# Kernel optimization log

Measured on AMD Instinct MI355X. Metric: run time of the kernel, lower is better.

## Reference

```python
import jax, jax.numpy as jnp
import numpy as np

B, LQ, LA = 128, 128, 512
VOCAB, EMB, FILT, K = 50000, 300, 400, 3
EPS = 1e-8


def setup_inputs() -> dict:
    key = jax.random.key(0)
    kq, ka, ke, kw, kb, kW = jax.random.split(key, 6)
    questions = jax.random.randint(kq, (B, LQ), 0, VOCAB + 1, dtype=jnp.int32)
    answers = jax.random.randint(ka, (B, LA), 0, VOCAB + 1, dtype=jnp.int32)
    emb = jax.random.normal(ke, (VOCAB + 1, EMB), dtype=jnp.float32) * 0.1
    emb = emb.at[0].set(0.0)  # padding_idx=0
    fan_in = EMB * K
    bound = 1.0 / np.sqrt(fan_in)
    conv_w = jax.random.uniform(kw, (FILT, EMB, K), jnp.float32, -bound, bound)
    conv_b = jax.random.uniform(kb, (FILT,), jnp.float32, -bound, bound)
    W = jax.random.normal(kW, (FILT, FILT), dtype=jnp.float32)  # init.normal_(std=1)
    return {"questions": questions, "answers": answers, "emb": emb,
            "conv_w": conv_w, "conv_b": conv_b, "W": W}


def _encode(tokens, emb, conv_w, conv_b):
    # tokens [B,L] -> embed [B,L,E] -> transpose to NCH [B,E,L] -> conv1d pad=1
    x = emb[tokens].transpose(0, 2, 1)
    y = jax.lax.conv_general_dilated(
        x, conv_w, window_strides=(1,), padding=[(1, 1)],
        dimension_numbers=("NCH", "OIH", "NCH"))
    return y + conv_b[None, :, None]  # [B, FILT, L]


def reference(questions, answers, emb, conv_w, conv_b, W):
    Q = _encode(questions, emb, conv_w, conv_b)  # [B,F,Lq]
    A = _encode(answers, emb, conv_w, conv_b)    # [B,F,La]
    # G = tanh(Q^T W A)  -> [B, Lq, La]
    G = jnp.tanh(jnp.einsum("bfq,fg,bga->bqa", Q, W, A))
    roQ = jax.nn.softmax(jnp.max(G, axis=2), axis=1)  # [B,Lq]
    roA = jax.nn.softmax(jnp.max(G, axis=1), axis=1)  # [B,La]
    rQ = jnp.einsum("bfq,bq->bf", Q, roQ)  # [B,F]
    rA = jnp.einsum("bfa,ba->bf", A, roA)  # [B,F]
    nQ = jnp.maximum(jnp.linalg.norm(rQ, axis=1), EPS)
    nA = jnp.maximum(jnp.linalg.norm(rA, axis=1), EPS)
    return jnp.sum(rQ * rA, axis=1) / (nQ * nA)  # [B]
```

## Files before the change

### kernel.cpp

```cpp
#include <hip/hip_runtime.h>
#include <hip/hip_bf16.h>

#define BB   128
#define LQ   128
#define LA   512
#define EMBD 300
#define FILT 400
#define KW   3

#define NT   25
#define KC   30
#define KCF  13
#define MT   32

typedef unsigned short u16;
typedef unsigned int   u32;
typedef __attribute__((ext_vector_type(4))) int    i32x4;
typedef __attribute__((ext_vector_type(4))) float  f32x4;
typedef __attribute__((ext_vector_type(8))) __bf16 bf16x8;

__device__ __forceinline__ u16 f2b(float f){
  u32 u = __float_as_uint(f);
  u32 r = (u + 0x7FFFu + ((u >> 16) & 1u)) >> 16;
  return (u16)r;
}
__device__ __forceinline__ u32 encf(float f){
  u32 u = __float_as_uint(f);
  return (u & 0x80000000u) ? ~u : (u | 0x80000000u);
}
__device__ __forceinline__ float decf(u32 k){
  u32 u = (k & 0x80000000u) ? (k ^ 0x80000000u) : ~k;
  return __uint_as_float(u);
}
__device__ __forceinline__ bf16x8 bzero(){
  i32x4 z; z.x = 0; z.y = 0; z.z = 0; z.w = 0;
  return __builtin_bit_cast(bf16x8, z);
}

__global__ void k_prep(const float* __restrict__ cw, const float* __restrict__ W,
                       u32* __restrict__ wTf, u32* __restrict__ wF){
  int idx = blockIdx.x * 256 + threadIdx.x;
  const int N1 = KC * NT * 64;
  const int N2 = KCF * NT * 64;
  if (idx < N1){
    int kc  = idx / (NT * 64);
    int rem = idx - kc * (NT * 64);
    int nt  = rem >> 6;
    int lane = rem & 63;
    int n = nt * 16 + (lane & 15);
    int quad = lane >> 4;
    u32 pack[4];
    #pragma unroll
    for (int d = 0; d < 4; d++){
      u16 h[2];
      #pragma unroll
      for (int s = 0; s < 2; s++){
        int kp = kc * 32 + quad * 8 + 2 * d + s;
        int kk = kp / 320, e = kp - kk * 320;
        float v = (e < EMBD) ? cw[(size_t)n * (EMBD * KW) + e * KW + kk] : 0.f;
        h[s] = f2b(v);
      }
      pack[d] = (u32)h[0] | ((u32)h[1] << 16);
    }
    i32x4 o; o.x = pack[0]; o.y = pack[1]; o.z = pack[2]; o.w = pack[3];
    *((i32x4*)wTf + idx) = o;
  } else if (idx < N1 + N2){
    int id2 = idx - N1;
    int kc  = id2 / (NT * 64);
    int rem = id2 - kc * (NT * 64);
    int nt  = rem >> 6;
    int lane = rem & 63;
    int n = nt * 16 + (lane & 15);
    int quad = lane >> 4;
    u32 pack[4];
    #pragma unroll
    for (int d = 0; d < 4; d++){
      u16 h[2];
      #pragma unroll
      for (int s = 0; s < 2; s++){
        int k = kc * 32 + quad * 8 + 2 * d + s;
        float v = (k < FILT) ? W[(size_t)k * FILT + n] : 0.f;
        h[s] = f2b(v);
      }
      pack[d] = (u32)h[0] | ((u32)h[1] << 16);
    }
    i32x4 o; o.x = pack[0]; o.y = pack[1]; o.z = pack[2]; o.w = pack[3];
    *((i32x4*)wF + id2) = o;
  }
}

__global__ __launch_bounds__(512) void k_encode_all(const int* __restrict__ qtok,
    const int* __restrict__ atok, const float* __restrict__ emb,
    const u32* __restrict__ wTf, const float* __restrict__ bias,
    u16* __restrict__ outQ, u16* __restrict__ outA){
  __shared__ u16 At[34 * 328];

  const int tid  = threadIdx.x;
  const int w    = tid >> 6;
  const int lane = tid & 63;
  const int col  = lane & 15;
  const int quad = lane >> 4;
  const int w4   = w & 3;
  const int half = w >> 2;
  const int base_nt = half ? 13 : 0;
  const bool has4 = (w == 0);
  const int nA = BB * LA / MT;
  const bool isA = ((int)blockIdx.x < nA);
  const int bi = isA ? blockIdx.x : (blockIdx.x - nA);
  const int L  = isA ? LA : LQ;
  const int* toks = isA ? atok : qtok;
  u16* out = isA ? outA : outQ;
  const int row0 = bi * MT;
  const int b    = row0 / L;
  const int l0   = row0 - b * L;

  int tk[5], cc[5], rws[5];
  #pragma unroll
  for (int u = 0; u < 5; u++){
    int idx = tid + 512 * u;
    tk[u] = -1; cc[u] = 0; rws[u] = 0;
    if (idx < 34 * 75){
      int r = idx / 75, c4 = idx - r * 75;
      int pos = l0 - 1 + r;
      cc[u] = c4;
      rws[u] = (r * 328 + c4 * 4) >> 1;
      if ((unsigned)pos < (unsigned)L) tk[u] = toks[b * L + pos];
    }
  }
  for (int i = tid; i < 34 * 328 / 2; i += 512) ((u32*)At)[i] = 0u;
  __syncthreads();
  {
    const float4* emb4 = (const float4*)emb;
    float4 v[5];
    #pragma unroll
    for (int u = 0; u < 5; u++)
      if (tk[u] >= 0) v[u] = emb4[(size_t)tk[u] * 75 + cc[u]];
    #pragma unroll
    for (int u = 0; u < 5; u++){
      if (tk[u] >= 0){
        u32 p0 = (u32)f2b(v[u].x) | ((u32)f2b(v[u].y) << 16);
        u32 p1 = (u32)f2b(v[u].z) | ((u32)f2b(v[u].w) << 16);
        ((u32*)At)[rws[u]]     = p0;
        ((u32*)At)[rws[u] + 1] = p1;
      }
    }
  }

  f32x4 acc[4][2];
  #pragma unroll
  for (int j = 0; j < 4; j++)
    #pragma unroll
    for (int mf = 0; mf < 2; mf++)
      acc[j][mf] = (f32x4){0.f, 0.f, 0.f, 0.f};

  __syncthreads();

  const i32x4* bbase = (const i32x4*)wTf + (size_t)(base_nt + w4) * 64 + lane;
  i32x4 Bb[2][4];
  i32x4 Ab[2][2];
  {
    #pragma unroll
    for (int j = 0; j < 3; j++) Bb[0][j] = bbase[(4 * j) * 64];
    if (has4) Bb[0][3] = bbase[12 * 64];
    const int ebase0 = quad * 8;
    Ab[0][0] = *(const i32x4*)(At + (col) * 328 + ebase0);
    Ab[0][1] = *(const i32x4*)(At + (16 + col) * 328 + ebase0);
  }
  #pragma unroll
  for (int kc = 0; kc < KC; kc++){
    const int cur = kc & 1;
    if (kc + 1 < KC){
      const i32x4* s = bbase + (size_t)(kc + 1) * (NT * 64);
      #pragma unroll
      for (int j = 0; j < 3; j++) Bb[cur ^ 1][j] = s[(4 * j) * 64];
      if (has4) Bb[cur ^ 1][3] = s[12 * 64];
      const int kk1 = (kc + 1) / 10, e01 = ((kc + 1) - kk1 * 10) * 32;
      const int ebase1 = e01 + quad * 8;
      Ab[cur ^ 1][0] = *(const i32x4*)(At + (col + kk1) * 328 + ebase1);
      Ab[cur ^ 1][1] = *(const i32x4*)(At + (16 + col + kk1) * 328 + ebase1);
    }
    bf16x8 a0 = __builtin_bit_cast(bf16x8, Ab[cur][0]);
    bf16x8 a1 = __builtin_bit_cast(bf16x8, Ab[cur][1]);
    #pragma unroll
    for (int j = 0; j < 3; j++){
      bf16x8 bf = __builtin_bit_cast(bf16x8, Bb[cur][j]);
      acc[j][0] = __builtin_amdgcn_mfma_f32_16x16x32_bf16(a0, bf, acc[j][0], 0, 0, 0);
      acc[j][1] = __builtin_amdgcn_mfma_f32_16x16x32_bf16(a1, bf, acc[j][1], 0, 0, 0);
    }
    if (has4){
      bf16x8 bf = __builtin_bit_cast(bf16x8, Bb[cur][3]);
      acc[3][0] = __builtin_amdgcn_mfma_f32_16x16x32_bf16(a0, bf, acc[3][0], 0, 0, 0);
      acc[3][1] = __builtin_amdgcn_mfma_f32_16x16x32_bf16(a1, bf, acc[3][1], 0, 0, 0);
    }
  }

  #pragma unroll
  for (int j = 0; j < 4; j++){
    if (j == 3 && !has4) continue;
    int n = ((j < 3) ? (base_nt + w4 + 4 * j) : 12) * 16 + col;
    float bv = bias[n];
    #pragma unroll
    for (int mf = 0; mf < 2; mf++){
      int rbase = row0 + mf * 16 + quad * 4;
      #pragma unroll
      for (int r = 0; r < 4; r++)
        out[(size_t)(rbase + r) * FILT + n] = f2b(acc[j][mf][r] + bv);
    }
  }
}

__global__ __launch_bounds__(512) void k_mid(const u16* __restrict__ QT,
    const u32* __restrict__ wF, const u16* __restrict__ AT,
    u32* __restrict__ rme, u32* __restrict__ cme){
  __shared__ u16 Ts[64 * 408];
  __shared__ float cpart[512][5];
  const int tid  = threadIdx.x;
  const int w    = tid >> 6;
  const int lane = tid & 63;
  const int col  = lane & 15;
  const int quad = lane >> 4;
  const int qh   = blockIdx.x;
  const int b    = blockIdx.y;
  const int wq   = w & 3;
  const int wh   = w >> 2;

  {
    const int bnt = wh ? 13 : 0;
    const int cnt = wh ? 12 : 13;
    const u16* arow = QT + (size_t)(b * LQ + qh * 64 + wq * 16 + col) * FILT;
    const i32x4* wFp = (const i32x4*)wF;
    for (int ntc = 0; ntc < 3; ntc++){
      const int nleft = cnt - ntc * 5;
      f32x4 acc[5];
      #pragma unroll
      for (int j = 0; j < 5; j++) acc[j] = (f32x4){0.f, 0.f, 0.f, 0.f};
      i32x4 Ab[2], Bb[2][5];
      Ab[0] = *(const i32x4*)(arow + quad * 8);
      #pragma unroll
      for (int j = 0; j < 5; j++)
        if (j < nleft) Bb[0][j] = wFp[(size_t)(bnt + ntc * 5 + j) * 64 + lane];
      for (int kc = 0; kc < KCF; kc++){
        const int cur = kc & 1;
        if (kc + 1 < KCF){
          Ab[cur ^ 1] = *(const i32x4*)(arow + (kc + 1) * 32 + quad * 8);
          #pragma unroll
          for (int j = 0; j < 5; j++)
            if (j < nleft)
              Bb[cur ^ 1][j] = wFp[((size_t)(kc + 1) * NT + bnt + ntc * 5 + j) * 64 + lane];
        }
        bf16x8 a = __builtin_bit_cast(bf16x8, Ab[cur]);
        #pragma unroll
        for (int j = 0; j < 5; j++)
          if (j < nleft)
            acc[j] = __builtin_amdgcn_mfma_f32_16x16x32_bf16(a,
                       __builtin_bit_cast(bf16x8, Bb[cur][j]), acc[j], 0, 0, 0);
      }
      #pragma unroll
      for (int j = 0; j < 5; j++){
        if (j < nleft){
          int g = (bnt + ntc * 5 + j) * 16 + col;
          #pragma unroll
          for (int r = 0; r < 4; r++)
            Ts[(wq * 16 + quad * 4 + r) * 408 + g] = f2b(acc[j][r]);
        }
      }
    }
  }
  __syncthreads();

  float rm[4];
  #pragma unroll
  for (int r = 0; r < 4; r++) rm[r] = -3.4e38f;
  const u16* Tsrow = Ts + (wq * 16 + col) * 408;
  for (int atg = 0; atg < 2; atg++){
    f32x4 acc[8];
    #pragma unroll
    for (int i = 0; i < 8; i++) acc[i] = (f32x4){0.f, 0.f, 0.f, 0.f};
    const u16* ar = AT + (size_t)(b * LA + wh * 256 + atg * 128 + col) * FILT;
    i32x4 Ab2[2], Bb2[2][8];
    Ab2[0] = *(const i32x4*)(Tsrow + quad * 8);
    #pragma unroll
    for (int i = 0; i < 8; i++)
      Bb2[0][i] = *(const i32x4*)(ar + (size_t)(i * 16) * FILT + quad * 8);
    for (int kc = 0; kc < KCF; kc++){
      const int cur = kc & 1;
      if (kc + 1 < KCF){
        int off = (kc + 1) * 32 + quad * 8;
        Ab2[cur ^ 1] = *(const i32x4*)(Tsrow + off);
        #pragma unroll
        for (int i = 0; i < 8; i++)
          Bb2[cur ^ 1][i] = *(const i32x4*)(ar + (size_t)(i * 16) * FILT + off);
      }
      const bool live = (kc < 12) || (quad < 2);
      bf16x8 a = live ? __builtin_bit_cast(bf16x8, Ab2[cur]) : bzero();
      #pragma unroll
      for (int i = 0; i < 8; i++)
        acc[i] = __builtin_amdgcn_mfma_f32_16x16x32_bf16(a,
                   __builtin_bit_cast(bf16x8, Bb2[cur][i]), acc[i], 0, 0, 0);
    }
    #pragma unroll
    for (int i = 0; i < 8; i++){
      float cmx = fmaxf(fmaxf(acc[i][0], acc[i][1]), fmaxf(acc[i][2], acc[i][3]));
      cmx = fmaxf(cmx, __shfl_xor(cmx, 16));
      cmx = fmaxf(cmx, __shfl_xor(cmx, 32));
      if (quad == 0) cpart[wh * 256 + atg * 128 + i * 16 + col][wq] = cmx;
      #pragma unroll
      for (int r = 0; r < 4; r++) rm[r] = fmaxf(rm[r], acc[i][r]);
    }
  }
  #pragma unroll
  for (int r = 0; r < 4; r++){
    float m = rm[r];
    m = fmaxf(m, __shfl_xor(m, 1));
    m = fmaxf(m, __shfl_xor(m, 2));
    m = fmaxf(m, __shfl_xor(m, 4));
    m = fmaxf(m, __shfl_xor(m, 8));
    if (col == 0)
      atomicMax(&rme[b * LQ + qh * 64 + wq * 16 + quad * 4 + r], encf(m));
  }
  __syncthreads();
  {
    float m = cpart[tid][0];
    #pragma unroll
    for (int s = 1; s < 4; s++) m = fmaxf(m, cpart[tid][s]);
    atomicMax(&cme[b * LA + tid], encf(m));
  }
}

__global__ __launch_bounds__(256) void k_pool(const u16* __restrict__ QT,
    const u16* __restrict__ AT, const u32* __restrict__ rme,
    const u32* __restrict__ cme, float* __restrict__ rqp, float* __restrict__ rap){
  __shared__ float sq[128];
  __shared__ float sa[512];
  __shared__ float red[4];
  const int s = blockIdx.x, b = blockIdx.y, tid = threadIdx.x;
  if (tid < 128) sq[tid] = tanhf(decf(rme[b * LQ + tid]));
  sa[tid]       = tanhf(decf(cme[b * LA + tid]));
  sa[tid + 256] = tanhf(decf(cme[b * LA + 256 + tid]));
  __syncthreads();
  if (tid < 64){
    float m = fmaxf(sq[tid], sq[tid + 64]);
    #pragma unroll
    for (int off = 32; off; off >>= 1) m = fmaxf(m, __shfl_down(m, off));
    if (tid == 0) red[0] = m;
  } else if (tid < 128){
    int l = tid - 64;
    float m = sa[l];
    #pragma unroll
    for (int i = 1; i < 8; i++) m = fmaxf(m, sa[l + 64 * i]);
    #pragma unroll
    for (int off = 32; off; off >>= 1) m = fmaxf(m, __shfl_down(m, off));
    if (l == 0) red[1] = m;
  }
  __syncthreads();
  if (tid < 128) sq[tid] = __expf(sq[tid] - red[0]);
  sa[tid]       = __expf(sa[tid] - red[1]);
  sa[tid + 256] = __expf(sa[tid + 256] - red[1]);
  __syncthreads();
  if (tid < 64){
    float v = sq[tid] + sq[tid + 64];
    #pragma unroll
    for (int off = 32; off; off >>= 1) v += __shfl_down(v, off);
    if (tid == 0) red[2] = v;
  } else if (tid < 128){
    int l = tid - 64;
    float v = 0.f;
    #pragma unroll
    for (int i = 0; i < 8; i++) v += sa[l + 64 * i];
    #pragma unroll
    for (int off = 32; off; off >>= 1) v += __shfl_down(v, off);
    if (l == 0) red[3] = v;
  }
  __syncthreads();
  if (tid < 128) sq[tid] *= (1.f / red[2]);
  sa[tid]       *= (1.f / red[3]);
  sa[tid + 256] *= (1.f / red[3]);
  __syncthreads();
  if (tid < FILT / 2){
    const u32* qp = (const u32*)(QT + (size_t)(b * LQ + s * 32) * FILT) + tid;
    const u32* ap = (const u32*)(AT + (size_t)(b * LA + s * 128) * FILT) + tid;
    float rq0 = 0.f, rq1 = 0.f, ra0 = 0.f, ra1 = 0.f;
    for (int q = 0; q < 32; q++){
      u32 u = qp[q * (FILT / 2)];
      float wv = sq[s * 32 + q];
      rq0 += __uint_as_float(u << 16) * wv;
      rq1 += __uint_as_float(u & 0xFFFF0000u) * wv;
    }
    for (int a = 0; a < 128; a++){
      u32 u = ap[a * (FILT / 2)];
      float wv = sa[s * 128 + a];
      ra0 += __uint_as_float(u << 16) * wv;
      ra1 += __uint_as_float(u & 0xFFFF0000u) * wv;
    }
    size_t base = ((size_t)b * 4 + s) * FILT + 2 * tid;
    rqp[base] = rq0; rqp[base + 1] = rq1;
    rap[base] = ra0; rap[base + 1] = ra1;
  }
}

__global__ __launch_bounds__(256) void k_cos(const float* __restrict__ rqp,
    const float* __restrict__ rap, float* __restrict__ outp){
  __shared__ float rd[4], r1[4], r2[4];
  int b = blockIdx.x, tid = threadIdx.x;
  int lane = tid & 63, w = tid >> 6;
  float d = 0.f, n1 = 0.f, n2 = 0.f;
  for (int f = tid; f < FILT; f += 256){
    size_t base = (size_t)b * 4 * FILT + f;
    float rq = rqp[base] + rqp[base + FILT] + rqp[base + 2 * FILT] + rqp[base + 3 * FILT];
    float ra = rap[base] + rap[base + FILT] + rap[base + 2 * FILT] + rap[base + 3 * FILT];
    d += rq * ra; n1 += rq * rq; n2 += ra * ra;
  }
  #pragma unroll
  for (int off = 32; off; off >>= 1){
    d  += __shfl_down(d, off);
    n1 += __shfl_down(n1, off);
    n2 += __shfl_down(n2, off);
  }
  if (lane == 0){ rd[w] = d; r1[w] = n1; r2[w] = n2; }
  __syncthreads();
  if (tid == 0){
    float D  = rd[0] + rd[1] + rd[2] + rd[3];
    float N1 = r1[0] + r1[1] + r1[2] + r1[3];
    float N2 = r2[0] + r2[1] + r2[2] + r2[3];
    outp[b] = D / (fmaxf(sqrtf(N1), 1e-8f) * fmaxf(sqrtf(N2), 1e-8f));
  }
}

extern "C" void kernel_launch(void* const* d_in, const int* in_sizes, int n_in,
                              void* d_out, int out_size, void* d_ws, size_t ws_size,
                              hipStream_t stream){
  const int*   qtok = (const int*)d_in[0];
  const int*   atok = (const int*)d_in[1];
  const float* emb  = (const float*)d_in[2];
  const float* cw   = (const float*)d_in[3];
  const float* cb   = (const float*)d_in[4];
  const float* W    = (const float*)d_in[5];
  float* outp = (float*)d_out;

  char* ws = (char*)d_ws;
  size_t off = 0;
  auto alloc = [&](size_t bytes) -> char* {
    char* p = ws + off;
    off = (off + bytes + 255) & ~(size_t)255;
    return p;
  };
  u32*   wTf = (u32*)alloc((size_t)KC * NT * 64 * 16);
  u32*   wF  = (u32*)alloc((size_t)KCF * NT * 64 * 16);
  u16*   QT  = (u16*)alloc((size_t)BB * LQ * FILT * 2);
  u16*   AT  = (u16*)alloc((size_t)BB * LA * FILT * 2);
  u32*   rme = (u32*)alloc((size_t)BB * LQ * 4);
  u32*   cme = (u32*)alloc((size_t)BB * LA * 4);
  float* rqp = (float*)alloc((size_t)BB * 4 * FILT * 4);
  float* rap = (float*)alloc((size_t)BB * 4 * FILT * 4);

  hipMemsetAsync(rme, 0, (size_t)BB * LQ * 4 + (size_t)BB * LA * 4, stream);

  const int NPREP = KC * NT * 64 + KCF * NT * 64;
  const int nA = BB * LA / MT;
  const int nQ = BB * LQ / MT;
  k_prep<<<dim3((NPREP + 255) / 256), 256, 0, stream>>>(cw, W, wTf, wF);
  k_encode_all<<<dim3(nA + nQ), 512, 0, stream>>>(qtok, atok, emb, wTf, cb, QT, AT);
  k_mid<<<dim3(2, BB), 512, 0, stream>>>(QT, wF, AT, rme, cme);
  k_pool<<<dim3(4, BB), 256, 0, stream>>>(QT, AT, rme, cme, rqp, rap);
  k_cos<<<dim3(BB), 256, 0, stream>>>(rqp, rap, outp);
}
```

Baseline: 248.6 us.

## Double encode row tile to 64 and give each wave full filter set

The conv encode kernel now handles 64 sequence rows per block instead of 32. Each of the 8 waves covers all 25 filter tiles, using tiles w, w+8, w+16 plus tile 24 on wave 0, across four 16-row fragments, instead of the old two halves of the filter range. This halves how often each block streams the packed weight matrix and improves MFMA reuse of every loaded B fragment. In exchange it uses more LDS and registers per block (launch_bounds hints 4 blocks), launches half as many blocks, and drops the A-fragment prefetch double buffering.

```diff
diff --git a/kernel.cpp b/kernel.cpp
--- a/kernel.cpp
+++ b/kernel.cpp
@@ -11,7 +11,7 @@
 #define NT   25
 #define KC   30
 #define KCF  13
-#define MT   32
+#define MT   64
 
 typedef unsigned short u16;
 typedef unsigned int   u32;
@@ -89,20 +89,17 @@
   }
 }
 
-__global__ __launch_bounds__(512) void k_encode_all(const int* __restrict__ qtok,
+__global__ __launch_bounds__(512, 4) void k_encode_all(const int* __restrict__ qtok,
     const int* __restrict__ atok, const float* __restrict__ emb,
     const u32* __restrict__ wTf, const float* __restrict__ bias,
     u16* __restrict__ outQ, u16* __restrict__ outA){
-  __shared__ u16 At[34 * 328];
+  __shared__ u16 At[66 * 328];
 
   const int tid  = threadIdx.x;
   const int w    = tid >> 6;
   const int lane = tid & 63;
   const int col  = lane & 15;
   const int quad = lane >> 4;
-  const int w4   = w & 3;
-  const int half = w >> 2;
-  const int base_nt = half ? 13 : 0;
   const bool has4 = (w == 0);
   const int nA = BB * LA / MT;
   const bool isA = ((int)blockIdx.x < nA);
@@ -114,12 +111,12 @@
   const int b    = row0 / L;
   const int l0   = row0 - b * L;
 
-  int tk[5], cc[5], rws[5];
-  #pragma unroll
-  for (int u = 0; u < 5; u++){
+  int tk[10], cc[10], rws[10];
+  #pragma unroll
+  for (int u = 0; u < 10; u++){
     int idx = tid + 512 * u;
     tk[u] = -1; cc[u] = 0; rws[u] = 0;
-    if (idx < 34 * 75){
+    if (idx < 66 * 75){
       int r = idx / 75, c4 = idx - r * 75;
       int pos = l0 - 1 + r;
       cc[u] = c4;
@@ -127,80 +124,84 @@
       if ((unsigned)pos < (unsigned)L) tk[u] = toks[b * L + pos];
     }
   }
-  for (int i = tid; i < 34 * 328 / 2; i += 512) ((u32*)At)[i] = 0u;
+  for (int i = tid; i < 66 * 328 / 2; i += 512) ((u32*)At)[i] = 0u;
   __syncthreads();
   {
     const float4* emb4 = (const float4*)emb;
-    float4 v[5];
-    #pragma unroll
-    for (int u = 0; u < 5; u++)
-      if (tk[u] >= 0) v[u] = emb4[(size_t)tk[u] * 75 + cc[u]];
-    #pragma unroll
-    for (int u = 0; u < 5; u++){
-      if (tk[u] >= 0){
-        u32 p0 = (u32)f2b(v[u].x) | ((u32)f2b(v[u].y) << 16);
-        u32 p1 = (u32)f2b(v[u].z) | ((u32)f2b(v[u].w) << 16);
-        ((u32*)At)[rws[u]]     = p0;
-        ((u32*)At)[rws[u] + 1] = p1;
-      }
-    }
-  }
-
-  f32x4 acc[4][2];
+    #pragma unroll
+    for (int g = 0; g < 2; g++){
+      float4 v[5];
+      #pragma unroll
+      for (int u = 0; u < 5; u++){
+        int uu = g * 5 + u;
+        if (tk[uu] >= 0) v[u] = emb4[(size_t)tk[uu] * 75 + cc[uu]];
+      }
+      #pragma unroll
+      for (int u = 0; u < 5; u++){
+        int uu = g * 5 + u;
+        if (tk[uu] >= 0){
+          u32 p0 = (u32)f2b(v[u].x) | ((u32)f2b(v[u].y) << 16);
+          u32 p1 = (u32)f2b(v[u].z) | ((u32)f2b(v[u].w) << 16);
+          ((u32*)At)[rws[uu]]     = p0;
+          ((u32*)At)[rws[uu] + 1] = p1;
+        }
+      }
+    }
+  }
+
+  f32x4 acc[4][4];
   #pragma unroll
   for (int j = 0; j < 4; j++)
     #pragma unroll
-    for (int mf = 0; mf < 2; mf++)
+    for (int mf = 0; mf < 4; mf++)
       acc[j][mf] = (f32x4){0.f, 0.f, 0.f, 0.f};
 
   __syncthreads();
 
-  const i32x4* bbase = (const i32x4*)wTf + (size_t)(base_nt + w4) * 64 + lane;
+  const i32x4* wTfp = (const i32x4*)wTf;
   i32x4 Bb[2][4];
-  i32x4 Ab[2][2];
   {
     #pragma unroll
-    for (int j = 0; j < 3; j++) Bb[0][j] = bbase[(4 * j) * 64];
-    if (has4) Bb[0][3] = bbase[12 * 64];
-    const int ebase0 = quad * 8;
-    Ab[0][0] = *(const i32x4*)(At + (col) * 328 + ebase0);
-    Ab[0][1] = *(const i32x4*)(At + (16 + col) * 328 + ebase0);
+    for (int j = 0; j < 3; j++) Bb[0][j] = wTfp[(size_t)(w + 8 * j) * 64 + lane];
+    if (has4) Bb[0][3] = wTfp[(size_t)24 * 64 + lane];
   }
   #pragma unroll
   for (int kc = 0; kc < KC; kc++){
     const int cur = kc & 1;
     if (kc + 1 < KC){
-      const i32x4* s = bbase + (size_t)(kc + 1) * (NT * 64);
-      #pragma unroll
-      for (int j = 0; j < 3; j++) Bb[cur ^ 1][j] = s[(4 * j) * 64];
-      if (has4) Bb[cur ^ 1][3] = s[12 * 64];
-      const int kk1 = (kc + 1) / 10, e01 = ((kc + 1) - kk1 * 10) * 32;
-      const int ebase1 = e01 + quad * 8;
-      Ab[cur ^ 1][0] = *(const i32x4*)(At + (col + kk1) * 328 + ebase1);
-      Ab[cur ^ 1][1] = *(const i32x4*)(At + (16 + col + kk1) * 328 + ebase1);
-    }
-    bf16x8 a0 = __builtin_bit_cast(bf16x8, Ab[cur][0]);
-    bf16x8 a1 = __builtin_bit_cast(bf16x8, Ab[cur][1]);
+      const i32x4* s = wTfp + (size_t)(kc + 1) * (NT * 64) + lane;
+      #pragma unroll
+      for (int j = 0; j < 3; j++) Bb[cur ^ 1][j] = s[(w + 8 * j) * 64];
+      if (has4) Bb[cur ^ 1][3] = s[24 * 64];
+    }
+    const int kk = kc / 10, e0 = (kc - kk * 10) * 32;
+    const int ebase = e0 + quad * 8;
+    bf16x8 a[4];
+    #pragma unroll
+    for (int mf = 0; mf < 4; mf++)
+      a[mf] = __builtin_bit_cast(bf16x8, *(const i32x4*)(At + (mf * 16 + col + kk) * 328 + ebase));
     #pragma unroll
     for (int j = 0; j < 3; j++){
       bf16x8 bf = __builtin_bit_cast(bf16x8, Bb[cur][j]);
-      acc[j][0] = __builtin_amdgcn_mfma_f32_16x16x32_bf16(a0, bf, acc[j][0], 0, 0, 0);
-      acc[j][1] = __builtin_amdgcn_mfma_f32_16x16x32_bf16(a1, bf, acc[j][1], 0, 0, 0);
+      #pragma unroll
+      for (int mf = 0; mf < 4; mf++)
+        acc[j][mf] = __builtin_amdgcn_mfma_f32_16x16x32_bf16(a[mf], bf, acc[j][mf], 0, 0, 0);
     }
     if (has4){
       bf16x8 bf = __builtin_bit_cast(bf16x8, Bb[cur][3]);
-      acc[3][0] = __builtin_amdgcn_mfma_f32_16x16x32_bf16(a0, bf, acc[3][0], 0, 0, 0);
-      acc[3][1] = __builtin_amdgcn_mfma_f32_16x16x32_bf16(a1, bf, acc[3][1], 0, 0, 0);
+      #pragma unroll
+      for (int mf = 0; mf < 4; mf++)
+        acc[3][mf] = __builtin_amdgcn_mfma_f32_16x16x32_bf16(a[mf], bf, acc[3][mf], 0, 0, 0);
     }
   }
 
   #pragma unroll
   for (int j = 0; j < 4; j++){
     if (j == 3 && !has4) continue;
-    int n = ((j < 3) ? (base_nt + w4 + 4 * j) : 12) * 16 + col;
+    int n = ((j < 3) ? (w + 8 * j) : 24) * 16 + col;
     float bv = bias[n];
     #pragma unroll
-    for (int mf = 0; mf < 2; mf++){
+    for (int mf = 0; mf < 4; mf++){
       int rbase = row0 + mf * 16 + quad * 4;
       #pragma unroll
       for (int r = 0; r < 4; r++)
```

Measured after the change: 234.6 us. 1.06x faster.
